# Performance work log

Hardware: AMD Instinct MI355X
Metric: run time of the kernel (lower is better)

## Reference

```python
import jax, jax.numpy as jnp
import numpy as np

B, H, L, D = 8, 8, 2048, 64
FACTOR = 5


def _num_sel(length):
    return min(int(FACTOR * np.ceil(np.log(length))), length)


def setup_inputs() -> dict:
    key = jax.random.key(0)
    kq, kk, kv, ki = jax.random.split(key, 4)
    num_k = _num_sel(L)
    return {
        "q": jax.random.normal(kq, (B, H, L, D), dtype=jnp.float32),
        "k": jax.random.normal(kk, (B, H, L, D), dtype=jnp.float32),
        "v": jax.random.normal(kv, (B, H, L, D), dtype=jnp.float32),
        "random_index": jax.random.randint(ki, (L, num_k), 0, L, dtype=jnp.int32),
    }


def reference(q, k, v, random_index):
    b, h, q_len, d = q.shape
    k_len = k.shape[2]
    num_q = _num_sel(q_len)

    # --- random K sampling per query: k_s[b,h,i,j,:] = k[b,h,random_index[i,j],:]
    k_s = k[:, :, random_index, :]                      # (B,H,L,num_k,D)
    pre_attn = jnp.einsum('bhid,bhijd->bhij', q, k_s)   # (B,H,L,num_k)
    measure = pre_attn.max(-1) - pre_attn.sum(-1) / k_len  # (B,H,L)

    # --- top-k query selection (sorted=False in torch; order-insensitive math)
    _, idx = jax.lax.top_k(measure, num_q)              # (B,H,num_q)
    q_sel = jnp.take_along_axis(q, idx[..., None], axis=2)  # (B,H,num_q,D)

    # --- reduced attention over all keys
    attn = jnp.einsum('bhid,bhjd->bhij', q_sel, k) * (d ** -0.5)  # (B,H,num_q,k_len)

    # ProbMask: causal mask per selected query index (mask where j > idx[i])
    mask = jnp.arange(k_len)[None, None, None, :] > idx[..., None]
    attn = jnp.where(mask, -jnp.inf, attn)
    attn = jax.nn.softmax(attn, axis=-1)

    out_sel = jnp.einsum('bhij,bhjd->bhid', attn, v)    # (B,H,num_q,D)

    # --- context initialization (use_mask=True branch) and scatter back
    context = jnp.cumsum(v, axis=2)                     # (B,H,L,D)
    bi = jnp.arange(b)[:, None, None]
    hi = jnp.arange(h)[None, :, None]
    out = context.at[bi, hi, idx].set(out_sel)          # (B,H,L,D)
    return out, attn
```

## Files before the change

### kernel.cpp

```cpp
#include <hip/hip_runtime.h>
#include <float.h>
#include <math.h>

#define B_  8
#define H_  8
#define L_  2048
#define D_  64
#define NS  40
#define BH  (B_*H_)
#define SCALE 0.125f


template<int CTRL>
__device__ __forceinline__ float dpp_add(float x) {
    int s = __builtin_amdgcn_update_dpp(0, __float_as_int(x), CTRL, 0xF, 0xF, true);
    return x + __int_as_float(s);
}

__global__ __launch_bounds__(256) void measure_kernel(
    const float* __restrict__ q, const float* __restrict__ k,
    const int* __restrict__ ridx, float* __restrict__ measure)
{
    int wave = threadIdx.x >> 6, lane = threadIdx.x & 63;
    int b = blockIdx.x;
    int xcd = b & 7, s = b >> 3;
    int bh  = xcd + ((s >> 9) << 3);
    int i   = (s & 511) * 4 + wave;
    int oct = lane >> 3;
    int e   = lane & 7;

    int4 r4 = *(const int4*)(ridx + i * NS + oct * 4);
    int  r5 = ridx[i * NS + 32 + oct];
    int rr[5] = { r4.x, r4.y, r4.z, r4.w, r5 };

    const float4* kb = (const float4*)(k + (size_t)bh * L_ * D_);
    const float4* qp = (const float4*)(q + ((size_t)bh * L_ + i) * D_);
    float4 qa = qp[e];
    float4 qb = qp[e + 8];

    float mx = -FLT_MAX, sm = 0.f;
    #pragma unroll
    for (int p = 0; p < 5; ++p) {
        int base = rr[p] << 4;
        float4 ka = kb[base + e];
        float4 kc = kb[base + 8 + e];
        float pa = qa.x*ka.x + qa.y*ka.y + qa.z*ka.z + qa.w*ka.w;
        float pb = qb.x*kc.x + qb.y*kc.y + qb.z*kc.z + qb.w*kc.w;
        float pp = pa + pb;
        pp = dpp_add<0x111>(pp);
        pp = dpp_add<0x112>(pp);
        pp = dpp_add<0x114>(pp);
        mx = fmaxf(mx, pp);
        sm += pp;
    }
    mx = fmaxf(mx, __shfl_xor(mx,  8, 64));  sm += __shfl_xor(sm,  8, 64);
    mx = fmaxf(mx, __shfl_xor(mx, 16, 64));  sm += __shfl_xor(sm, 16, 64);
    mx = fmaxf(mx, __shfl_xor(mx, 32, 64));  sm += __shfl_xor(sm, 32, 64);
    if (lane == 7)
        measure[(size_t)bh * L_ + i] = mx - sm * (1.0f / (float)L_);
}

__global__ __launch_bounds__(256) void topk_kernel(
    const float* __restrict__ measure, int* __restrict__ idxOut)
{
    __shared__ float segVal[4][NS];
    __shared__ int   segIdx[4][NS];
    int bh = blockIdx.x;
    int t = threadIdx.x, w = t >> 6, lane = t & 63;
    const float4* m4 = (const float4*)(measure + (size_t)bh * L_);

    float vals[8];
    float4 a  = m4[128*w + 2*lane];
    float4 bb = m4[128*w + 2*lane + 1];
    vals[0]=a.x;  vals[1]=a.y;  vals[2]=a.z;  vals[3]=a.w;
    vals[4]=bb.x; vals[5]=bb.y; vals[6]=bb.z; vals[7]=bb.w;
    int gbase = 512*w + 8*lane;

    float lv = -FLT_MAX; int li = 0x7fffffff;
    #pragma unroll
    for (int e = 0; e < 8; ++e)
        if (vals[e] > lv) { lv = vals[e]; li = gbase + e; }

    for (int r = 0; r < NS; ++r) {
        float v = lv; int idx = li;
        #pragma unroll
        for (int off = 32; off; off >>= 1) {
            float ov = __shfl_xor(v, off, 64);
            int   oi = __shfl_xor(idx, off, 64);
            if (ov > v || (ov == v && oi < idx)) { v = ov; idx = oi; }
        }
        if (lane == 0) { segVal[w][r] = v; segIdx[w][r] = idx; }
        if (((idx >> 3) & 63) == lane) {
            int slot = idx & 7;
            #pragma unroll
            for (int e = 0; e < 8; ++e) if (e == slot) vals[e] = -FLT_MAX;
            lv = -FLT_MAX; li = 0x7fffffff;
            #pragma unroll
            for (int e = 0; e < 8; ++e)
                if (vals[e] > lv) { lv = vals[e]; li = gbase + e; }
        }
    }
    __syncthreads();

    if (w == 0) {
        int s = lane & 3;
        int h = 0;
        float hv = segVal[s][0]; int hi_ = segIdx[s][0];
        for (int r = 0; r < NS; ++r) {
            float v = hv; int idx = hi_; int ws = s;
            float ov = __shfl_xor(v, 1, 64); int oi = __shfl_xor(idx, 1, 64); int os = __shfl_xor(ws, 1, 64);
            if (ov > v || (ov == v && oi < idx)) { v = ov; idx = oi; ws = os; }
            ov = __shfl_xor(v, 2, 64); oi = __shfl_xor(idx, 2, 64); os = __shfl_xor(ws, 2, 64);
            if (ov > v || (ov == v && oi < idx)) { v = ov; idx = oi; ws = os; }
            if (lane == 0) idxOut[bh*NS + r] = idx;
            if (s == ws) {
                ++h;
                if (h < NS) { hv = segVal[s][h]; hi_ = segIdx[s][h]; }
                else        { hv = -FLT_MAX;     hi_ = 0x7fffffff;  }
            }
        }
    }
}

__global__ __launch_bounds__(256) void cumsum_fused(
    const float* __restrict__ v, float* __restrict__ out)
{
    __shared__ float4 part[64][5];
    int b = blockIdx.x;
    int xcd = b & 7, s = b >> 3;
    int bh  = xcd + ((s >> 2) << 3);
    int cg  = s & 3;
    int col = threadIdx.x & 3, sub = threadIdx.x >> 2;
    int c0 = cg*4 + col;
    int r0 = sub * 32;
    const float4* vb = (const float4*)(v + (size_t)bh * L_ * D_);
    float4*       ob = (float4*)(out + (size_t)bh * L_ * D_);

    float4 acc = make_float4(0,0,0,0);
    #pragma unroll
    for (int r = 0; r < 32; ++r) {
        float4 x = vb[(size_t)(r0 + r)*16 + c0];
        acc.x += x.x; acc.y += x.y; acc.z += x.z; acc.w += x.w;
    }
    part[sub][col] = acc;
    __syncthreads();

    float4 run = make_float4(0,0,0,0);
    for (int cc = 0; cc < sub; ++cc) {
        float4 x = part[cc][col];
        run.x += x.x; run.y += x.y; run.z += x.z; run.w += x.w;
    }

    #pragma unroll
    for (int r = 0; r < 32; ++r) {
        float4 x = vb[(size_t)(r0 + r)*16 + c0];
        run.x += x.x; run.y += x.y; run.z += x.z; run.w += x.w;
        ob[(size_t)(r0 + r)*16 + c0] = run;
    }
}

__global__ __launch_bounds__(256) void scores_kernel(
    const float* __restrict__ q, const float* __restrict__ k,
    const int* __restrict__ idxSel, float* __restrict__ attn)
{
    __shared__ float4 kbuf[16 * 129];
    int b = blockIdx.x;
    int xcd = b & 7, s = b >> 3;
    int bh  = xcd + ((s / 10) << 3);
    int grp = s % 10;
    int qi = threadIdx.x >> 6, sub = threadIdx.x & 63;
    int rank = grp*4 + qi;
    int qrow = idxSel[bh*NS + rank];

    const float4* qrp = (const float4*)(q + ((size_t)bh * L_ + qrow) * D_);
    float4 qreg[16];
    #pragma unroll
    for (int g = 0; g < 16; ++g) qreg[g] = qrp[g];

    const float4* kb = (const float4*)(k + (size_t)bh * L_ * D_);
    float sc0[16], sc1[16];

    #pragma unroll
    for (int c = 0; c < 16; ++c) {
        __syncthreads();
        int j0 = c * 128;
        #pragma unroll
        for (int it = 0; it < 8; ++it) {
            int fi = threadIdx.x + 256*it;
            int g = fi & 15, j = fi >> 4;
            kbuf[g*129 + j] = kb[(size_t)(j0 + j)*16 + g];
        }
        __syncthreads();
        float acc0 = 0.f, acc1 = 0.f;
        #pragma unroll
        for (int g = 0; g < 16; ++g) {
            float4 k0 = kbuf[g*129 + sub];
            float4 k1 = kbuf[g*129 + sub + 64];
            float4 qq = qreg[g];
            acc0 += qq.x*k0.x + qq.y*k0.y + qq.z*k0.z + qq.w*k0.w;
            acc1 += qq.x*k1.x + qq.y*k1.y + qq.z*k1.z + qq.w*k1.w;
        }
        sc0[c] = acc0 * SCALE;
        sc1[c] = acc1 * SCALE;
    }

    float mx = -FLT_MAX;
    #pragma unroll
    for (int c = 0; c < 16; ++c) {
        if (c*128 + sub      <= qrow) mx = fmaxf(mx, sc0[c]);
        if (c*128 + sub + 64 <= qrow) mx = fmaxf(mx, sc1[c]);
    }
    #pragma unroll
    for (int off = 32; off; off >>= 1) mx = fmaxf(mx, __shfl_xor(mx, off, 64));

    float sum = 0.f;
    #pragma unroll
    for (int c = 0; c < 16; ++c) {
        sc0[c] = (c*128 + sub      <= qrow) ? __expf(sc0[c] - mx) : 0.f;
        sc1[c] = (c*128 + sub + 64 <= qrow) ? __expf(sc1[c] - mx) : 0.f;
        sum += sc0[c] + sc1[c];
    }
    #pragma unroll
    for (int off = 32; off; off >>= 1) sum += __shfl_xor(sum, off, 64);
    float inv = 1.f / sum;

    float* arow = attn + (size_t)(bh*NS + rank) * L_;
    #pragma unroll
    for (int c = 0; c < 16; ++c) {
        arow[c*128 + sub]      = sc0[c] * inv;
        arow[c*128 + sub + 64] = sc1[c] * inv;
    }
}

__global__ __launch_bounds__(256) void pv_kernel(
    const float* __restrict__ v, const int* __restrict__ idxSel,
    const float* __restrict__ attn, float* __restrict__ out)
{
    __shared__ float wl[4][L_ + 64];
    __shared__ float4 part[16][16];
    __shared__ int qr4[4];
    int b = blockIdx.x;
    int xcd = b & 7, s = b >> 3;
    int bh  = xcd + ((s / 10) << 3);
    int grp = s % 10;
    int t = threadIdx.x;
    if (t < 4) qr4[t] = idxSel[bh*NS + grp*4 + t];

    #pragma unroll
    for (int it = 0; it < 8; ++it) {
        int f = t + 256*it;
        int rr = f >> 9, fi = f & 511;
        const float4* ar = (const float4*)(attn + (size_t)(bh*NS + grp*4 + rr) * L_);
        float4 x = ar[fi];
        int j = 4*fi;
        *((float4*)&wl[rr][j + 4*(j >> 7)]) = x;
    }
    __syncthreads();

    int maxq = max(max(qr4[0], qr4[1]), max(qr4[2], qr4[3]));
    int d4 = t & 15, seg = t >> 4;
    const float4* vb = (const float4*)(v + (size_t)bh * L_ * D_);
    float4 acc[4];
    #pragma unroll
    for (int rr = 0; rr < 4; ++rr) acc[rr] = make_float4(0,0,0,0);

    int jlo = seg*128, jhi = min(jlo + 127, maxq);
    for (int j = jlo; j <= jhi; ++j) {
        float4 x = vb[(size_t)j*16 + d4];
        int jp = j + 4*(j >> 7);
        #pragma unroll
        for (int rr = 0; rr < 4; ++rr) {
            float wgt = wl[rr][jp];
            acc[rr].x += wgt*x.x; acc[rr].y += wgt*x.y;
            acc[rr].z += wgt*x.z; acc[rr].w += wgt*x.w;
        }
    }

    #pragma unroll
    for (int rr = 0; rr < 4; ++rr) {
        part[seg][d4] = acc[rr];
        __syncthreads();
        float4 a = acc[rr];
        for (int s2 = 8; s2; s2 >>= 1) {
            if (seg < s2) {
                float4 o = part[seg + s2][d4];
                a.x += o.x; a.y += o.y; a.z += o.z; a.w += o.w;
                part[seg][d4] = a;
            }
            __syncthreads();
        }
        if (seg == 0) {
            float4* orow = (float4*)(out + ((size_t)bh * L_ + qr4[rr]) * D_);
            orow[d4] = a;
        }
        __syncthreads();
    }
}

extern "C" void kernel_launch(void* const* d_in, const int* in_sizes, int n_in,
                              void* d_out, int out_size, void* d_ws, size_t ws_size,
                              hipStream_t stream) {
    const float* q    = (const float*)d_in[0];
    const float* k    = (const float*)d_in[1];
    const float* v    = (const float*)d_in[2];
    const int*   ridx = (const int*)d_in[3];

    float* out     = (float*)d_out;
    float* attnOut = out + (size_t)BH * L_ * D_;

    float*  measure = (float*)d_ws;
    int*    idxSel  = (int*)((char*)d_ws + (size_t)BH * L_ * sizeof(float));

    measure_kernel<<<BH * L_ / 4, 256, 0, stream>>>(q, k, ridx, measure);
    topk_kernel   <<<BH,          256, 0, stream>>>(measure, idxSel);
    cumsum_fused  <<<BH * 4,      256, 0, stream>>>(v, out);
    scores_kernel <<<BH * 10,     256, 0, stream>>>(q, k, idxSel, attnOut);
    pv_kernel     <<<BH * 10,     256, 0, stream>>>(v, idxSel, attnOut, out);
}
```

Measured before the change: 325.0 us.

## Stage K tiles in shared memory for measure kernel sampled dot products

Restructures the sparsity-measure kernel so each 512-thread block loads a 512-row K tile into LDS with a rotated layout and walks over four tiles. For each query it uses ballots to find which sampled keys fall in the current tile and computes only those dot products from LDS. This swaps scattered global gathers of K rows for coalesced tile loads plus LDS reads. The costs are a grid of only 256 blocks with 128KB LDS each, which lowers occupancy, and a serial per-query loop with divergent ballot iterations.

```diff
diff --git a/kernel.cpp b/kernel.cpp
--- a/kernel.cpp
+++ b/kernel.cpp
@@ -17,47 +17,71 @@
     return x + __int_as_float(s);
 }
 
-__global__ __launch_bounds__(256) void measure_kernel(
+__global__ __launch_bounds__(512) void measure_kernel(
     const float* __restrict__ q, const float* __restrict__ k,
     const int* __restrict__ ridx, float* __restrict__ measure)
 {
-    int wave = threadIdx.x >> 6, lane = threadIdx.x & 63;
+    __shared__ float4 kt[512 * 16];
+    int t = threadIdx.x;
+    int wv = t >> 6, lane = t & 63;
     int b = blockIdx.x;
     int xcd = b & 7, s = b >> 3;
-    int bh  = xcd + ((s >> 9) << 3);
-    int i   = (s & 511) * 4 + wave;
-    int oct = lane >> 3;
-    int e   = lane & 7;
-
-    int4 r4 = *(const int4*)(ridx + i * NS + oct * 4);
-    int  r5 = ridx[i * NS + 32 + oct];
-    int rr[5] = { r4.x, r4.y, r4.z, r4.w, r5 };
-
-    const float4* kb = (const float4*)(k + (size_t)bh * L_ * D_);
-    const float4* qp = (const float4*)(q + ((size_t)bh * L_ + i) * D_);
-    float4 qa = qp[e];
-    float4 qb = qp[e + 8];
-
-    float mx = -FLT_MAX, sm = 0.f;
-    #pragma unroll
-    for (int p = 0; p < 5; ++p) {
-        int base = rr[p] << 4;
-        float4 ka = kb[base + e];
-        float4 kc = kb[base + 8 + e];
-        float pa = qa.x*ka.x + qa.y*ka.y + qa.z*ka.z + qa.w*ka.w;
-        float pb = qb.x*kc.x + qb.y*kc.y + qb.z*kc.z + qb.w*kc.w;
-        float pp = pa + pb;
-        pp = dpp_add<0x111>(pp);
-        pp = dpp_add<0x112>(pp);
-        pp = dpp_add<0x114>(pp);
-        mx = fmaxf(mx, pp);
-        sm += pp;
-    }
-    mx = fmaxf(mx, __shfl_xor(mx,  8, 64));  sm += __shfl_xor(sm,  8, 64);
-    mx = fmaxf(mx, __shfl_xor(mx, 16, 64));  sm += __shfl_xor(sm, 16, 64);
-    mx = fmaxf(mx, __shfl_xor(mx, 32, 64));  sm += __shfl_xor(sm, 32, 64);
-    if (lane == 7)
-        measure[(size_t)bh * L_ + i] = mx - sm * (1.0f / (float)L_);
+    int bh  = xcd + ((s & 7) << 3);
+    int chunk = s >> 3;
+    int qbase = chunk * 512 + wv * 64;
+    int oct = lane >> 3, e = lane & 7;
+
+    const float4* kb  = (const float4*)(k + (size_t)bh * L_ * D_);
+    const float4* qb4 = (const float4*)(q + (size_t)bh * L_ * D_);
+
+    float mxq = -FLT_MAX, smq = 0.f;
+
+    for (int T = 0; T < 4; ++T) {
+        __syncthreads();
+        #pragma unroll
+        for (int it = 0; it < 16; ++it) {
+            int f = t + 512*it;
+            int row = f >> 4, j = f & 15;
+            kt[row*16 + ((j + row) & 15)] = kb[(size_t)(T*512 + row)*16 + j];
+        }
+        __syncthreads();
+
+        for (int qq = 0; qq < 64; ++qq) {
+            int i = qbase + qq;
+            int rl = ridx[i * NS + (lane < NS ? lane : NS - 1)];
+            unsigned long long M = __ballot((lane < NS) && ((rl >> 9) == T));
+            float4 qa = qb4[(size_t)i*16 + e];
+            float4 qc = qb4[(size_t)i*16 + e + 8];
+            unsigned long long m = M;
+            #pragma unroll
+            for (int c = 0; c < 7; ++c) if (c < oct) m &= m - 1;
+
+            float mxt = -FLT_MAX, smt = 0.f;
+            while (__ballot(m != 0ULL)) {
+                bool valid = (m != 0ULL);
+                int pos = valid ? ((int)__ffsll((long long)m) - 1) : 0;
+                int r  = __shfl(rl, pos, 64);
+                int lr = r & 511;
+                float4 ka = kt[lr*16 + ((e + lr) & 15)];
+                float4 kc = kt[lr*16 + ((e + 8 + lr) & 15)];
+                float pp = qa.x*ka.x + qa.y*ka.y + qa.z*ka.z + qa.w*ka.w
+                         + qc.x*kc.x + qc.y*kc.y + qc.z*kc.z + qc.w*kc.w;
+                pp = dpp_add<0x111>(pp);
+                pp = dpp_add<0x112>(pp);
+                pp = dpp_add<0x114>(pp);
+                if (valid) { mxt = fmaxf(mxt, pp); smt += pp; }
+                #pragma unroll
+                for (int c = 0; c < 8; ++c) m &= m - 1;
+            }
+            mxt = fmaxf(mxt, __shfl_xor(mxt,  8, 64)); smt += __shfl_xor(smt,  8, 64);
+            mxt = fmaxf(mxt, __shfl_xor(mxt, 16, 64)); smt += __shfl_xor(smt, 16, 64);
+            mxt = fmaxf(mxt, __shfl_xor(mxt, 32, 64)); smt += __shfl_xor(smt, 32, 64);
+            float bmx = __shfl(mxt, 7, 64);
+            float bsm = __shfl(smt, 7, 64);
+            if (lane == qq) { mxq = fmaxf(mxq, bmx); smq += bsm; }
+        }
+    }
+    measure[(size_t)bh * L_ + qbase + lane] = mxq - smq * (1.0f / (float)L_);
 }
 
 __global__ __launch_bounds__(256) void topk_kernel(
@@ -311,9 +335,9 @@
     float*  measure = (float*)d_ws;
     int*    idxSel  = (int*)((char*)d_ws + (size_t)BH * L_ * sizeof(float));
 
-    measure_kernel<<<BH * L_ / 4, 256, 0, stream>>>(q, k, ridx, measure);
-    topk_kernel   <<<BH,          256, 0, stream>>>(measure, idxSel);
-    cumsum_fused  <<<BH * 4,      256, 0, stream>>>(v, out);
-    scores_kernel <<<BH * 10,     256, 0, stream>>>(q, k, idxSel, attnOut);
-    pv_kernel     <<<BH * 10,     256, 0, stream>>>(v, idxSel, attnOut, out);
-}
+    measure_kernel<<<256,        512, 0, stream>>>(q, k, ridx, measure);
+    topk_kernel   <<<BH,         256, 0, stream>>>(measure, idxSel);
+    cumsum_fused  <<<BH * 4,     256, 0, stream>>>(v, out);
+    scores_kernel <<<BH * 10,    256, 0, stream>>>(q, k, idxSel, attnOut);
+    pv_kernel     <<<BH * 10,    256, 0, stream>>>(v, idxSel, attnOut, out);
+}
```

After: 505.7 us. 55.6% more time.
